# Kernel optimization log

Measured on AMD Instinct MI355X. Metric: run time of the kernel, lower is better.

Reference implementation:

```python
import jax, jax.numpy as jnp
import numpy as np

LATENT_DIM = 512
BATCH = 1024


def setup_inputs() -> dict:
    key = jax.random.key(0)
    k1, k2 = jax.random.split(key)
    ctrl_latent = jax.random.normal(k1, (BATCH, LATENT_DIM), dtype=jnp.float32)
    weights = jax.random.normal(k2, (LATENT_DIM, LATENT_DIM), dtype=jnp.float32)
    bias = jnp.zeros((LATENT_DIM,), dtype=jnp.float32)
    return {"ctrl_latent": ctrl_latent, "weights": weights, "bias": bias}


def reference(ctrl_latent, weights, bias):
    # Math (eval mode, dropout = identity):
    #   pred[b, i] = sum_j x[b, i] * x[b, j] * W[i, j] + bias[i]
    # Fused form avoiding the (batch, d, d) intermediate:
    #   pred = x * (x @ W.T) + bias
    wx = jnp.einsum('bj,ij->bi', ctrl_latent, weights)  # (B, d)
    return ctrl_latent * wx + bias
```

## Files before the change

kernel.cpp:

```cpp
#include <hip/hip_runtime.h>
#include <stdint.h>


#define LATENT 512
#define BATCH  1024
#define XN (BATCH * LATENT)
#define WN (LATENT * LATENT)

typedef short bf16x8 __attribute__((ext_vector_type(8)));
typedef float f32x4  __attribute__((ext_vector_type(4)));

__device__ __forceinline__ short f2bf(float f) {
    uint32_t u = __builtin_bit_cast(uint32_t, f);
    u += 0x7FFFu + ((u >> 16) & 1u);
    return (short)(u >> 16);
}

__global__ __launch_bounds__(256) void convert_kernel(
    const float* __restrict__ X, const float* __restrict__ W,
    short* __restrict__ Xb, short* __restrict__ Wb)
{
    const int g = (blockIdx.x * 256 + threadIdx.x) * 8;
    const float* src;
    short* dst;
    if (g < XN) { src = X + g;        dst = Xb + g; }
    else        { src = W + (g - XN); dst = Wb + (g - XN); }
    f32x4 v0 = ((const f32x4*)src)[0];
    f32x4 v1 = ((const f32x4*)src)[1];
    short s[8];
    #pragma unroll
    for (int i = 0; i < 4; ++i) s[i]     = f2bf(v0[i]);
    #pragma unroll
    for (int i = 0; i < 4; ++i) s[4 + i] = f2bf(v1[i]);
    *(bf16x8*)dst = *(bf16x8*)s;
}

__global__ __launch_bounds__(64) void gemm_kernel(
    const short* __restrict__ Xb, const short* __restrict__ Wb,
    const float* __restrict__ X, const float* __restrict__ bias,
    float* __restrict__ out)
{
    const int lane = threadIdx.x;
    const int m0   = blockIdx.y * 32;
    const int n0   = blockIdx.x * 32;
    const int lrow = lane & 15;
    const int q    = lane >> 4;

    const short* ap0 = Xb + (size_t)(m0 + lrow) * LATENT + q * 8;
    const short* ap1 = ap0 + 16 * LATENT;
    const short* bp0 = Wb + (size_t)(n0 + lrow) * LATENT + q * 8;
    const short* bp1 = bp0 + 16 * LATENT;

    f32x4 acc[2][2] = {};
    #pragma unroll
    for (int ks = 0; ks < 16; ++ks) {
        bf16x8 a0 = *(const bf16x8*)(ap0 + ks * 32);
        bf16x8 a1 = *(const bf16x8*)(ap1 + ks * 32);
        bf16x8 b0 = *(const bf16x8*)(bp0 + ks * 32);
        bf16x8 b1 = *(const bf16x8*)(bp1 + ks * 32);
        acc[0][0] = __builtin_amdgcn_mfma_f32_16x16x32_bf16(a0, b0, acc[0][0], 0, 0, 0);
        acc[0][1] = __builtin_amdgcn_mfma_f32_16x16x32_bf16(a0, b1, acc[0][1], 0, 0, 0);
        acc[1][0] = __builtin_amdgcn_mfma_f32_16x16x32_bf16(a1, b0, acc[1][0], 0, 0, 0);
        acc[1][1] = __builtin_amdgcn_mfma_f32_16x16x32_bf16(a1, b1, acc[1][1], 0, 0, 0);
    }

    #pragma unroll
    for (int mi = 0; mi < 2; ++mi) {
        #pragma unroll
        for (int ni = 0; ni < 2; ++ni) {
            #pragma unroll
            for (int r = 0; r < 4; ++r) {
                const int m = m0 + mi * 16 + q * 4 + r;
                const int n = n0 + ni * 16 + lrow;
                out[(size_t)m * LATENT + n] =
                    X[(size_t)m * LATENT + n] * acc[mi][ni][r] + bias[n];
            }
        }
    }
}

extern "C" void kernel_launch(void* const* d_in, const int* in_sizes, int n_in,
                              void* d_out, int out_size, void* d_ws, size_t ws_size,
                              hipStream_t stream) {
    const float* X    = (const float*)d_in[0];
    const float* W    = (const float*)d_in[1];
    const float* bias = (const float*)d_in[2];
    float* out        = (float*)d_out;

    short* Xb = (short*)d_ws;
    short* Wb = (short*)d_ws + XN;

    convert_kernel<<<(XN + WN) / 8 / 256, 256, 0, stream>>>(X, W, Xb, Wb);
    gemm_kernel<<<dim3(LATENT / 32, BATCH / 32), 64, 0, stream>>>(Xb, Wb, X, bias, out);
}
```

Baseline: 64.59 us.

## Fuse bf16 conversion into GEMM and drop separate convert kernel

Removes the standalone fp32-to-bf16 conversion pass and workspace, instead loading fp32 X and W directly in the GEMM and converting in registers with the packed v_cvt_pk_bf16_f32 instruction. The tile is narrowed from 32x32 to 32x16 per wave, doubling the grid to give more blocks. This saves one kernel launch and the round trip through workspace memory. In exchange, each block reads twice the bytes (fp32), the same inputs are converted redundantly across blocks, and the smaller tile reduces reuse of X.

```diff
diff --git a/kernel.cpp b/kernel.cpp
--- a/kernel.cpp
+++ b/kernel.cpp
@@ -4,77 +4,60 @@
 
 #define LATENT 512
 #define BATCH  1024
-#define XN (BATCH * LATENT)
-#define WN (LATENT * LATENT)
 
 typedef short bf16x8 __attribute__((ext_vector_type(8)));
 typedef float f32x4  __attribute__((ext_vector_type(4)));
 
-__device__ __forceinline__ short f2bf(float f) {
-    uint32_t u = __builtin_bit_cast(uint32_t, f);
-    u += 0x7FFFu + ((u >> 16) & 1u);
-    return (short)(u >> 16);
+__device__ __forceinline__ int cvt_pk(float lo, float hi) {
+    int d;
+    asm("v_cvt_pk_bf16_f32 %0, %1, %2" : "=v"(d) : "v"(lo), "v"(hi));
+    return d;
 }
 
-__global__ __launch_bounds__(256) void convert_kernel(
-    const float* __restrict__ X, const float* __restrict__ W,
-    short* __restrict__ Xb, short* __restrict__ Wb)
-{
-    const int g = (blockIdx.x * 256 + threadIdx.x) * 8;
-    const float* src;
-    short* dst;
-    if (g < XN) { src = X + g;        dst = Xb + g; }
-    else        { src = W + (g - XN); dst = Wb + (g - XN); }
-    f32x4 v0 = ((const f32x4*)src)[0];
-    f32x4 v1 = ((const f32x4*)src)[1];
-    short s[8];
-    #pragma unroll
-    for (int i = 0; i < 4; ++i) s[i]     = f2bf(v0[i]);
-    #pragma unroll
-    for (int i = 0; i < 4; ++i) s[4 + i] = f2bf(v1[i]);
-    *(bf16x8*)dst = *(bf16x8*)s;
+__device__ __forceinline__ bf16x8 ld_cvt8(const float* __restrict__ p) {
+    f32x4 v0 = ((const f32x4*)p)[0];
+    f32x4 v1 = ((const f32x4*)p)[1];
+    union { int i[4]; bf16x8 v; } u;
+    u.i[0] = cvt_pk(v0[0], v0[1]);
+    u.i[1] = cvt_pk(v0[2], v0[3]);
+    u.i[2] = cvt_pk(v1[0], v1[1]);
+    u.i[3] = cvt_pk(v1[2], v1[3]);
+    return u.v;
 }
 
-__global__ __launch_bounds__(64) void gemm_kernel(
-    const short* __restrict__ Xb, const short* __restrict__ Wb,
-    const float* __restrict__ X, const float* __restrict__ bias,
-    float* __restrict__ out)
+__global__ __launch_bounds__(64) void fused_kernel(
+    const float* __restrict__ X, const float* __restrict__ W,
+    const float* __restrict__ bias, float* __restrict__ out)
 {
     const int lane = threadIdx.x;
+    const int n0   = blockIdx.x * 16;
     const int m0   = blockIdx.y * 32;
-    const int n0   = blockIdx.x * 32;
     const int lrow = lane & 15;
     const int q    = lane >> 4;
 
-    const short* ap0 = Xb + (size_t)(m0 + lrow) * LATENT + q * 8;
-    const short* ap1 = ap0 + 16 * LATENT;
-    const short* bp0 = Wb + (size_t)(n0 + lrow) * LATENT + q * 8;
-    const short* bp1 = bp0 + 16 * LATENT;
+    const float* ap0 = X + (size_t)(m0 + lrow) * LATENT + q * 8;
+    const float* ap1 = ap0 + 16 * LATENT;
+    const float* bp0 = W + (size_t)(n0 + lrow) * LATENT + q * 8;
 
-    f32x4 acc[2][2] = {};
+    f32x4 acc[2] = {};
     #pragma unroll
     for (int ks = 0; ks < 16; ++ks) {
-        bf16x8 a0 = *(const bf16x8*)(ap0 + ks * 32);
-        bf16x8 a1 = *(const bf16x8*)(ap1 + ks * 32);
-        bf16x8 b0 = *(const bf16x8*)(bp0 + ks * 32);
-        bf16x8 b1 = *(const bf16x8*)(bp1 + ks * 32);
-        acc[0][0] = __builtin_amdgcn_mfma_f32_16x16x32_bf16(a0, b0, acc[0][0], 0, 0, 0);
-        acc[0][1] = __builtin_amdgcn_mfma_f32_16x16x32_bf16(a0, b1, acc[0][1], 0, 0, 0);
-        acc[1][0] = __builtin_amdgcn_mfma_f32_16x16x32_bf16(a1, b0, acc[1][0], 0, 0, 0);
-        acc[1][1] = __builtin_amdgcn_mfma_f32_16x16x32_bf16(a1, b1, acc[1][1], 0, 0, 0);
+        bf16x8 a0 = ld_cvt8(ap0 + ks * 32);
+        bf16x8 a1 = ld_cvt8(ap1 + ks * 32);
+        bf16x8 b0 = ld_cvt8(bp0 + ks * 32);
+        acc[0] = __builtin_amdgcn_mfma_f32_16x16x32_bf16(a0, b0, acc[0], 0, 0, 0);
+        acc[1] = __builtin_amdgcn_mfma_f32_16x16x32_bf16(a1, b0, acc[1], 0, 0, 0);
     }
 
+    const float bv = bias[n0 + lrow];
     #pragma unroll
     for (int mi = 0; mi < 2; ++mi) {
         #pragma unroll
-        for (int ni = 0; ni < 2; ++ni) {
-            #pragma unroll
-            for (int r = 0; r < 4; ++r) {
-                const int m = m0 + mi * 16 + q * 4 + r;
-                const int n = n0 + ni * 16 + lrow;
-                out[(size_t)m * LATENT + n] =
-                    X[(size_t)m * LATENT + n] * acc[mi][ni][r] + bias[n];
-            }
+        for (int r = 0; r < 4; ++r) {
+            const int m = m0 + mi * 16 + q * 4 + r;
+            const int n = n0 + lrow;
+            out[(size_t)m * LATENT + n] =
+                X[(size_t)m * LATENT + n] * acc[mi][r] + bv;
         }
     }
 }
@@ -86,10 +69,7 @@
     const float* W    = (const float*)d_in[1];
     const float* bias = (const float*)d_in[2];
     float* out        = (float*)d_out;
+    (void)d_ws; (void)ws_size;
 
-    short* Xb = (short*)d_ws;
-    short* Wb = (short*)d_ws + XN;
-
-    convert_kernel<<<(XN + WN) / 8 / 256, 256, 0, stream>>>(X, W, Xb, Wb);
-    gemm_kernel<<<dim3(LATENT / 32, BATCH / 32), 64, 0, stream>>>(Xb, Wb, X, bias, out);
+    fused_kernel<<<dim3(LATENT / 16, BATCH / 32), 64, 0, stream>>>(X, W, bias, out);
 }
```

Result: slower. 69.04 us (+6.9%).
